# Optimization experiments

Measured on AMD Instinct MI355X. Metric: run time of the kernel, lower is better.

The kernel has to match this reference:

```python
import jax, jax.numpy as jnp
import numpy as np

GAM1 = 1.0
GAM2 = 1.0
EPS = 0.01


def setup_inputs() -> dict:
    key = jax.random.key(0)
    kx, ky = jax.random.split(key)
    m, p, k = 16384, 512, 10
    X = jax.random.normal(kx, (m, p), dtype=jnp.float32)
    Y = jax.random.randint(ky, (m,), 0, k, dtype=jnp.int64)
    return {"X": X, "Y": Y, "num_classes": k}


def reference(X, Y, num_classes):
    # W: [p, m] (features x samples), as in the torch module (W = X.T)
    W = X.reshape(X.shape[0], -1).T
    p, m = W.shape
    I = jnp.eye(p, dtype=W.dtype)

    # ---- empirical discriminative loss ----
    scalar = p / (m * EPS)
    G = W @ W.T  # [p, p]
    discrimn = jnp.linalg.slogdet(I + GAM1 * scalar * G)[1] / 2.0

    # ---- empirical compressive loss ----
    # Pi[j] is diagonal with the one-hot membership of class j, so
    # W @ Pi[j] @ W.T == (W * mask_j) @ W.T. Build all k masked Grams at once.
    M = jax.nn.one_hot(Y, num_classes, dtype=W.dtype)  # [m, k]
    trPi = M.sum(axis=0) + 1e-8                         # [k] class counts
    # Gk[j] = sum_{i in class j} w_i w_i^T  -> [k, p, p]
    Gk = jnp.einsum('pm,mk,qm->kpq', W, M, W)
    scal = (p / (trPi * EPS))[:, None, None]
    logdets = jnp.linalg.slogdet(I[None] + scal * Gk)[1]  # [k]
    compress = jnp.sum(logdets * trPi / m) / 2.0

    return (discrimn, compress)
```

## Files before the change

### kernel.cpp

```cpp
#include <hip/hip_runtime.h>
#include <math.h>

#define P 512
#define KC 10
#define NB 32
#define EPSV 0.01f
#define TR_ROWS 448
#define XT 17024
#define MSTRIDE 40

typedef __attribute__((ext_vector_type(8))) __bf16 bf16x8;
typedef __attribute__((ext_vector_type(4))) float floatx4;

__device__ __forceinline__ float rdl(float x, int l){
  return __builtin_bit_cast(float, __builtin_amdgcn_readlane(__builtin_bit_cast(int, x), l));
}

__global__ __launch_bounds__(256) void sort_k(const int* __restrict__ Y, int* __restrict__ colmap,
                                              int* __restrict__ counts, int* __restrict__ off_pad, int m){
  __shared__ int cnt[KC], offp[KC + 1], cur[KC];
  int tid = threadIdx.x;
  if (tid < KC) cnt[tid] = 0;
  __syncthreads();
  for (int i = tid; i < m; i += 256){
    int y = Y[i];
    if (y >= 0 && y < KC) atomicAdd(&cnt[y], 1);
  }
  __syncthreads();
  if (tid == 0){
    int s = 0;
    for (int j = 0; j < KC; ++j){ offp[j] = s; s += ((cnt[j] + 63) >> 6) << 6; }
    offp[KC] = s;
  }
  __syncthreads();
  if (tid < KC){ cur[tid] = offp[tid]; counts[tid] = cnt[tid]; off_pad[tid] = offp[tid]; }
  if (tid == KC) off_pad[KC] = offp[KC];
  for (int i = tid; i < XT; i += 256) colmap[i] = -1;
  __syncthreads();
  for (int i = tid; i < m; i += 256){
    int y = Y[i];
    if (y >= 0 && y < KC){
      int pos = atomicAdd(&cur[y], 1);
      colmap[pos] = i;
    }
  }
}

__global__ __launch_bounds__(256) void xt_k(const float* __restrict__ X, const int* __restrict__ colmap,
                                            __bf16* __restrict__ Xhi, __bf16* __restrict__ Xlo){
  __shared__ float T[64][65];
  int c0 = blockIdx.x * 64;
  int f0 = blockIdx.y * 64;
  int tid = threadIdx.x;

  int j = tid >> 2;
  int piece = tid & 3;
  int s = colmap[c0 + j];
  if (s >= 0){
    const float* src = X + (long)s * P + f0 + piece * 16;
    #pragma unroll
    for (int q = 0; q < 4; ++q){
      float4 v = *(const float4*)(src + q * 4);
      T[piece * 16 + q * 4 + 0][j] = v.x;
      T[piece * 16 + q * 4 + 1][j] = v.y;
      T[piece * 16 + q * 4 + 2][j] = v.z;
      T[piece * 16 + q * 4 + 3][j] = v.w;
    }
  } else {
    #pragma unroll
    for (int q = 0; q < 16; ++q) T[piece * 16 + q][j] = 0.f;
  }
  __syncthreads();

  int f = tid >> 2;
  int cp = (tid & 3) * 16;
  bf16x8 vh0, vl0, vh1, vl1;
  #pragma unroll
  for (int q = 0; q < 8; ++q){
    float x0 = T[f][cp + q];
    float x1 = T[f][cp + 8 + q];
    __bf16 h0 = (__bf16)x0, h1 = (__bf16)x1;
    vh0[q] = h0; vl0[q] = (__bf16)(x0 - (float)h0);
    vh1[q] = h1; vl1[q] = (__bf16)(x1 - (float)h1);
  }
  long base = (long)(f0 + f) * XT + c0 + cp;
  *(bf16x8*)&Xhi[base]     = vh0;
  *(bf16x8*)&Xhi[base + 8] = vh1;
  *(bf16x8*)&Xlo[base]     = vl0;
  *(bf16x8*)&Xlo[base + 8] = vl1;
}

__global__ __launch_bounds__(256) void gram_mfma(const __bf16* __restrict__ Xhi,
                                                 const __bf16* __restrict__ Xlo,
                                                 const int* __restrict__ counts,
                                                 const int* __restrict__ off_pad,
                                                 float* __restrict__ Gk){
  int cls = blockIdx.y;
  int ta = 0, rem = blockIdx.x;
  while (rem >= ta + 1){ rem -= ta + 1; ++ta; }
  int tb = rem;
  int a0 = ta * 64, b0 = tb * 64;

  int tid  = threadIdx.x;
  int lane = tid & 63;
  int wv   = tid >> 6;
  int wrow = wv >> 1, wcol = wv & 1;
  int fr   = lane & 15;
  int quad = lane >> 4;

  int cs0     = off_pad[cls];
  int nchunks = (counts[cls] + 31) >> 5;

  long arow0 = (long)(a0 + wrow * 32 + fr) * XT;
  long brow0 = (long)(b0 + wcol * 32 + fr) * XT;

  floatx4 acc[2][2];
  #pragma unroll
  for (int i = 0; i < 2; ++i)
    #pragma unroll
    for (int j = 0; j < 2; ++j) acc[i][j] = (floatx4){0.f, 0.f, 0.f, 0.f};

  for (int ch = 0; ch < nchunks; ++ch){
    long co = cs0 + ch * 32 + quad * 8;
    bf16x8 ah[2], al[2], bh[2], bl[2];
    #pragma unroll
    for (int r = 0; r < 2; ++r){
      ah[r] = *(const bf16x8*)&Xhi[arow0 + (long)r * 16 * XT + co];
      al[r] = *(const bf16x8*)&Xlo[arow0 + (long)r * 16 * XT + co];
      bh[r] = *(const bf16x8*)&Xhi[brow0 + (long)r * 16 * XT + co];
      bl[r] = *(const bf16x8*)&Xlo[brow0 + (long)r * 16 * XT + co];
    }
    #pragma unroll
    for (int ri = 0; ri < 2; ++ri)
      #pragma unroll
      for (int rj = 0; rj < 2; ++rj){
        acc[ri][rj] = __builtin_amdgcn_mfma_f32_16x16x32_bf16(al[ri], bh[rj], acc[ri][rj], 0, 0, 0);
        acc[ri][rj] = __builtin_amdgcn_mfma_f32_16x16x32_bf16(ah[ri], bl[rj], acc[ri][rj], 0, 0, 0);
        acc[ri][rj] = __builtin_amdgcn_mfma_f32_16x16x32_bf16(ah[ri], bh[rj], acc[ri][rj], 0, 0, 0);
      }
  }

  float* C = Gk + (long)cls * P * P;
  #pragma unroll
  for (int ri = 0; ri < 2; ++ri){
    int a = a0 + wrow * 32 + ri * 16 + (lane >> 4) * 4;
    #pragma unroll
    for (int rj = 0; rj < 2; ++rj){
      int b = b0 + wcol * 32 + rj * 16 + (lane & 15);
      #pragma unroll
      for (int r = 0; r < 4; ++r)
        C[(long)(a + r) * P + b] = acc[ri][rj][r];
    }
  }
}

__global__ __launch_bounds__(256) void sum10_k(float* __restrict__ Gk){
  long i = (long)blockIdx.x * 256 + threadIdx.x;
  float4 s = {0.f, 0.f, 0.f, 0.f};
  #pragma unroll
  for (int j = 0; j < KC; ++j){
    float4 v = ((const float4*)(Gk + (long)j * P * P))[i];
    s.x += v.x; s.y += v.y; s.z += v.z; s.w += v.w;
  }
  ((float4*)(Gk + (long)KC * P * P))[i] = s;
}

__global__ __launch_bounds__(512, 2) void chol_mfma(float* __restrict__ Gk,
                                                    const int* __restrict__ counts,
                                                    float* __restrict__ logdets,
                                                    float m_tot){
  __shared__ __align__(16) __bf16 Lhi[TR_ROWS * 32];
  __shared__ __align__(16) __bf16 Llo[TR_ROWS * 32];
  __shared__ __align__(16) __bf16 Mhi[NB * MSTRIDE];
  __shared__ __align__(16) __bf16 Mlo[NB * MSTRIDE];

  int mat  = blockIdx.x;
  int tid  = threadIdx.x;
  int lane = tid & 63;
  int wv   = tid >> 6;
  float* A = Gk + (long)mat * P * P;
  float sc = (mat < KC) ? ((float)P / (((float)counts[mat] + 1e-8f) * EPSV))
                        : ((float)P / (m_tot * EPSV));
  float logsum = 0.f;

  for (int s = 0; s < 16; ++s){
    int j0 = s * NB;
    int qt = P - j0 - NB;

    if (wv == 0){
      float a[NB];
      float dri[NB];
      if (lane < NB){
        const float* src = A + (long)(j0 + lane) * P + j0;
        #pragma unroll
        for (int u = 0; u < NB; u += 4){
          float4 v = *(const float4*)(src + u);
          a[u] = v.x; a[u+1] = v.y; a[u+2] = v.z; a[u+3] = v.w;
        }
        if (s == 0){
          #pragma unroll
          for (int u = 0; u < NB; ++u) a[u] *= sc;
          a[lane] += 1.0f;
        }
      } else {
        #pragma unroll
        for (int u = 0; u < NB; ++u) a[u] = 0.f;
      }
      #pragma unroll
      for (int jj = 0; jj < NB; ++jj){
        float d = rdl(a[jj], jj);
        logsum += __log2f(d);
        float inv = 1.0f / d;
        float rs  = rsqrtf(d);
        dri[jj] = rs;
        float w = a[jj] * inv;
        #pragma unroll
        for (int l = jj + 1; l < NB; ++l){
          float prl = rdl(a[l], jj);
          a[l] = fmaf(-w, prl, a[l]);
        }
        a[jj] *= rs;
      }
      float mcol[NB];
      #pragma unroll
      for (int u = 0; u < NB; ++u) mcol[u] = 0.f;
      #pragma unroll
      for (int r = 0; r < NB; ++r){
        float ssum = (lane == r) ? 1.0f : 0.0f;
        #pragma unroll
        for (int u = 0; u < r; ++u){
          float lru = rdl(a[u], r);
          ssum = fmaf(-lru, mcol[u], ssum);
        }
        mcol[r] = ssum * dri[r];
      }
      if (lane < NB){
        #pragma unroll
        for (int u = 0; u < NB; ++u){
          float f = mcol[u];
          __bf16 h = (__bf16)f;
          Mhi[u * MSTRIDE + lane] = h;
          Mlo[u * MSTRIDE + lane] = (__bf16)(f - (float)h);
        }
      }
    }
    __syncthreads();

    if (qt > 0){
      int ntiles = qt >> 4;
      int r16 = lane & 15;
      int kq  = lane >> 4;
      for (int rt = wv; rt < ntiles; rt += 8){
        int row = j0 + NB + rt * 16 + r16;
        const float* src = A + (long)row * P + j0 + kq * 8;
        float4 v0 = *(const float4*)(src);
        float4 v1 = *(const float4*)(src + 4);
        float f[8] = {v0.x, v0.y, v0.z, v0.w, v1.x, v1.y, v1.z, v1.w};
        if (s == 0){
          #pragma unroll
          for (int u = 0; u < 8; ++u) f[u] *= sc;
        }
        bf16x8 ahi, alo;
        #pragma unroll
        for (int u = 0; u < 8; ++u){
          __bf16 h = (__bf16)f[u];
          ahi[u] = h;
          alo[u] = (__bf16)(f[u] - (float)h);
        }
        #pragma unroll
        for (int ng = 0; ng < 2; ++ng){
          int mrow = ng * 16 + r16;
          bf16x8 bhi = *(const bf16x8*)&Mhi[mrow * MSTRIDE + kq * 8];
          bf16x8 blo = *(const bf16x8*)&Mlo[mrow * MSTRIDE + kq * 8];
          floatx4 acc = {0.f, 0.f, 0.f, 0.f};
          acc = __builtin_amdgcn_mfma_f32_16x16x32_bf16(alo, bhi, acc, 0, 0, 0);
          acc = __builtin_amdgcn_mfma_f32_16x16x32_bf16(ahi, blo, acc, 0, 0, 0);
          acc = __builtin_amdgcn_mfma_f32_16x16x32_bf16(ahi, bhi, acc, 0, 0, 0);
          #pragma unroll
          for (int r = 0; r < 4; ++r){
            int t  = rt * 16 + kq * 4 + r;
            int cc = ng * 16 + r16;
            int e  = (t * 4 + ((cc >> 3) ^ ((t >> 1) & 3))) * 8 + (cc & 7);
            float fv = acc[r];
            __bf16 h = (__bf16)fv;
            Lhi[e] = h;
            Llo[e] = (__bf16)(fv - (float)h);
          }
        }
      }
    }
    __syncthreads();

    if (qt > 0){
      int tt = qt >> 5;
      int T  = tt * (tt + 1) / 2;
      int trail0 = j0 + NB;
      for (int idx = wv; idx < T; idx += 8){
        int ti = 0, rem = idx;
        while (rem >= ti + 1){ rem -= ti + 1; ++ti; }
        int tj = rem;
        int I0 = ti * 32, J0 = tj * 32;
        int c  = lane >> 4;

        bf16x8 ahi2[2], alo2[2], bhi2[2], blo2[2];
        #pragma unroll
        for (int h = 0; h < 2; ++h){
          int r1 = I0 + h * 16 + (lane & 15);
          int sw1 = (r1 * 4 + (c ^ ((r1 >> 1) & 3))) * 8;
          ahi2[h] = *(const bf16x8*)&Lhi[sw1];
          alo2[h] = *(const bf16x8*)&Llo[sw1];
          int r2 = J0 + h * 16 + (lane & 15);
          int sw2 = (r2 * 4 + (c ^ ((r2 >> 1) & 3))) * 8;
          bhi2[h] = *(const bf16x8*)&Lhi[sw2];
          blo2[h] = *(const bf16x8*)&Llo[sw2];
        }

        #pragma unroll
        for (int hi_ = 0; hi_ < 2; ++hi_){
          #pragma unroll
          for (int hj = 0; hj < 2; ++hj){
            floatx4 acc = {0.f, 0.f, 0.f, 0.f};
            acc = __builtin_amdgcn_mfma_f32_16x16x32_bf16(alo2[hi_], bhi2[hj], acc, 0, 0, 0);
            acc = __builtin_amdgcn_mfma_f32_16x16x32_bf16(ahi2[hi_], blo2[hj], acc, 0, 0, 0);
            acc = __builtin_amdgcn_mfma_f32_16x16x32_bf16(ahi2[hi_], bhi2[hj], acc, 0, 0, 0);
            int grow0 = trail0 + I0 + hi_ * 16 + (lane >> 4) * 4;
            int gcol  = trail0 + J0 + hj  * 16 + (lane & 15);
            #pragma unroll
            for (int r = 0; r < 4; ++r){
              long off = (long)(grow0 + r) * P + gcol;
              float v = A[off];
              if (s == 0) v = sc * v + ((grow0 + r) == gcol ? 1.f : 0.f);
              A[off] = v - acc[r];
            }
          }
        }
      }
    }
    __syncthreads();
  }

  if (tid == 0) logdets[mat] = logsum * 0.6931471805599453f;
}

__global__ __launch_bounds__(64) void final_k(const float* __restrict__ logdets,
                                              const int* __restrict__ counts,
                                              float* __restrict__ out, float m_tot){
  if (threadIdx.x == 0 && blockIdx.x == 0){
    out[0] = 0.5f * logdets[KC];
    float comp = 0.f;
    for (int j = 0; j < KC; ++j){
      float trPi = (float)counts[j] + 1e-8f;
      comp += logdets[j] * trPi / m_tot;
    }
    out[1] = 0.5f * comp;
  }
}

extern "C" void kernel_launch(void* const* d_in, const int* in_sizes, int n_in,
                              void* d_out, int out_size, void* d_ws, size_t ws_size,
                              hipStream_t stream) {
  (void)n_in; (void)out_size; (void)ws_size;
  const float* X = (const float*)d_in[0];
  const int*   Y = (const int*)d_in[1];
  int m = in_sizes[0] / P;

  float*  Gk      = (float*)d_ws;
  __bf16* Xhi     = (__bf16*)(Gk + 11L * P * P);
  __bf16* Xlo     = Xhi + (long)P * XT;
  int*    colmap  = (int*)(Xlo + (long)P * XT);
  int*    counts  = colmap + XT;
  int*    off_pad = counts + 16;
  float*  logdets = (float*)(off_pad + 17);

  sort_k<<<1, 256, 0, stream>>>(Y, colmap, counts, off_pad, m);

  dim3 xg(XT / 64, 8);
  xt_k<<<xg, 256, 0, stream>>>(X, colmap, Xhi, Xlo);

  dim3 gg(36, KC);
  gram_mfma<<<gg, 256, 0, stream>>>(Xhi, Xlo, counts, off_pad, Gk);

  sum10_k<<<P * P / 1024, 256, 0, stream>>>(Gk);

  chol_mfma<<<KC + 1, 512, 0, stream>>>(Gk, counts, logdets, (float)m);

  final_k<<<1, 64, 0, stream>>>(logdets, counts, (float*)d_out, (float)m);
}
```

Measured before the change: 503.3 us.

## Split blocked Cholesky into per-step panel and multi-block trailing update kernels

The single-kernel blocked Cholesky, which ran one workgroup per matrix, is replaced by a host loop over 16 steps. Each step launches a panel kernel that factors the diagonal block and computes the panel L into a global bf16 hi/lo scratch, then a trailing-update kernel that spreads the symmetric rank-32 update over 8 workgroups per matrix. This lifts parallelism from 11 workgroups to 88 for the dominant trailing update. In exchange it adds about 31 kernel launches, moves the panel through global memory instead of LDS, drops the LDS swizzle, and accumulates log-determinants across launches in a global buffer.

Result: slower. 530.5 us (+5.4%).

```diff
diff --git a/kernel.cpp b/kernel.cpp
--- a/kernel.cpp
+++ b/kernel.cpp
@@ -8,6 +8,7 @@
 #define TR_ROWS 448
 #define XT 17024
 #define MSTRIDE 40
+#define NBLK 8
 
 typedef __attribute__((ext_vector_type(8))) __bf16 bf16x8;
 typedef __attribute__((ext_vector_type(4))) float floatx4;
@@ -17,10 +18,12 @@
 }
 
 __global__ __launch_bounds__(256) void sort_k(const int* __restrict__ Y, int* __restrict__ colmap,
-                                              int* __restrict__ counts, int* __restrict__ off_pad, int m){
+                                              int* __restrict__ counts, int* __restrict__ off_pad,
+                                              float* __restrict__ logacc, int m){
   __shared__ int cnt[KC], offp[KC + 1], cur[KC];
   int tid = threadIdx.x;
   if (tid < KC) cnt[tid] = 0;
+  if (tid < 16) logacc[tid] = 0.f;
   __syncthreads();
   for (int i = tid; i < m; i += 256){
     int y = Y[i];
@@ -165,12 +168,11 @@
   ((float4*)(Gk + (long)KC * P * P))[i] = s;
 }
 
-__global__ __launch_bounds__(512, 2) void chol_mfma(float* __restrict__ Gk,
-                                                    const int* __restrict__ counts,
-                                                    float* __restrict__ logdets,
-                                                    float m_tot){
-  __shared__ __align__(16) __bf16 Lhi[TR_ROWS * 32];
-  __shared__ __align__(16) __bf16 Llo[TR_ROWS * 32];
+__global__ __launch_bounds__(512, 2) void panel_k(float* __restrict__ Gk,
+                                                  const int* __restrict__ counts,
+                                                  float* __restrict__ logacc,
+                                                  __bf16* __restrict__ Lsc,
+                                                  float m_tot, int s){
   __shared__ __align__(16) __bf16 Mhi[NB * MSTRIDE];
   __shared__ __align__(16) __bf16 Mlo[NB * MSTRIDE];
 
@@ -179,48 +181,51 @@
   int lane = tid & 63;
   int wv   = tid >> 6;
   float* A = Gk + (long)mat * P * P;
+  __bf16* Lh = Lsc + (long)mat * 2 * TR_ROWS * 32;
+  __bf16* Ll = Lh + TR_ROWS * 32;
   float sc = (mat < KC) ? ((float)P / (((float)counts[mat] + 1e-8f) * EPSV))
                         : ((float)P / (m_tot * EPSV));
-  float logsum = 0.f;
-
-  for (int s = 0; s < 16; ++s){
-    int j0 = s * NB;
-    int qt = P - j0 - NB;
-
-    if (wv == 0){
-      float a[NB];
-      float dri[NB];
-      if (lane < NB){
-        const float* src = A + (long)(j0 + lane) * P + j0;
-        #pragma unroll
-        for (int u = 0; u < NB; u += 4){
-          float4 v = *(const float4*)(src + u);
-          a[u] = v.x; a[u+1] = v.y; a[u+2] = v.z; a[u+3] = v.w;
-        }
-        if (s == 0){
-          #pragma unroll
-          for (int u = 0; u < NB; ++u) a[u] *= sc;
-          a[lane] += 1.0f;
-        }
-      } else {
-        #pragma unroll
-        for (int u = 0; u < NB; ++u) a[u] = 0.f;
-      }
-      #pragma unroll
-      for (int jj = 0; jj < NB; ++jj){
-        float d = rdl(a[jj], jj);
-        logsum += __log2f(d);
-        float inv = 1.0f / d;
-        float rs  = rsqrtf(d);
-        dri[jj] = rs;
-        float w = a[jj] * inv;
-        #pragma unroll
-        for (int l = jj + 1; l < NB; ++l){
-          float prl = rdl(a[l], jj);
-          a[l] = fmaf(-w, prl, a[l]);
-        }
-        a[jj] *= rs;
-      }
+
+  int j0 = s * NB;
+  int qt = P - j0 - NB;
+
+  if (wv == 0){
+    float a[NB];
+    float dri[NB];
+    float logsum = 0.f;
+    if (lane < NB){
+      const float* src = A + (long)(j0 + lane) * P + j0;
+      #pragma unroll
+      for (int u = 0; u < NB; u += 4){
+        float4 v = *(const float4*)(src + u);
+        a[u] = v.x; a[u+1] = v.y; a[u+2] = v.z; a[u+3] = v.w;
+      }
+      if (s == 0){
+        #pragma unroll
+        for (int u = 0; u < NB; ++u) a[u] *= sc;
+        a[lane] += 1.0f;
+      }
+    } else {
+      #pragma unroll
+      for (int u = 0; u < NB; ++u) a[u] = 0.f;
+    }
+    #pragma unroll
+    for (int jj = 0; jj < NB; ++jj){
+      float d = rdl(a[jj], jj);
+      logsum += __log2f(d);
+      float inv = 1.0f / d;
+      float rs  = rsqrtf(d);
+      dri[jj] = rs;
+      float w = a[jj] * inv;
+      #pragma unroll
+      for (int l = jj + 1; l < NB; ++l){
+        float prl = rdl(a[l], jj);
+        a[l] = fmaf(-w, prl, a[l]);
+      }
+      a[jj] *= rs;
+    }
+    if (lane == 0) logacc[mat] += logsum;
+    if (qt > 0){
       float mcol[NB];
       #pragma unroll
       for (int u = 0; u < NB; ++u) mcol[u] = 0.f;
@@ -244,113 +249,126 @@
         }
       }
     }
-    __syncthreads();
-
-    if (qt > 0){
-      int ntiles = qt >> 4;
-      int r16 = lane & 15;
-      int kq  = lane >> 4;
-      for (int rt = wv; rt < ntiles; rt += 8){
-        int row = j0 + NB + rt * 16 + r16;
-        const float* src = A + (long)row * P + j0 + kq * 8;
-        float4 v0 = *(const float4*)(src);
-        float4 v1 = *(const float4*)(src + 4);
-        float f[8] = {v0.x, v0.y, v0.z, v0.w, v1.x, v1.y, v1.z, v1.w};
-        if (s == 0){
-          #pragma unroll
-          for (int u = 0; u < 8; ++u) f[u] *= sc;
+  }
+  __syncthreads();
+
+  if (qt > 0){
+    int ntiles = qt >> 4;
+    int r16 = lane & 15;
+    int kq  = lane >> 4;
+    for (int rt = wv; rt < ntiles; rt += 8){
+      int row = j0 + NB + rt * 16 + r16;
+      const float* src = A + (long)row * P + j0 + kq * 8;
+      float4 v0 = *(const float4*)(src);
+      float4 v1 = *(const float4*)(src + 4);
+      float f[8] = {v0.x, v0.y, v0.z, v0.w, v1.x, v1.y, v1.z, v1.w};
+      if (s == 0){
+        #pragma unroll
+        for (int u = 0; u < 8; ++u) f[u] *= sc;
+      }
+      bf16x8 ahi, alo;
+      #pragma unroll
+      for (int u = 0; u < 8; ++u){
+        __bf16 h = (__bf16)f[u];
+        ahi[u] = h;
+        alo[u] = (__bf16)(f[u] - (float)h);
+      }
+      #pragma unroll
+      for (int ng = 0; ng < 2; ++ng){
+        int mrow = ng * 16 + r16;
+        bf16x8 bhi = *(const bf16x8*)&Mhi[mrow * MSTRIDE + kq * 8];
+        bf16x8 blo = *(const bf16x8*)&Mlo[mrow * MSTRIDE + kq * 8];
+        floatx4 acc = {0.f, 0.f, 0.f, 0.f};
+        acc = __builtin_amdgcn_mfma_f32_16x16x32_bf16(alo, bhi, acc, 0, 0, 0);
+        acc = __builtin_amdgcn_mfma_f32_16x16x32_bf16(ahi, blo, acc, 0, 0, 0);
+        acc = __builtin_amdgcn_mfma_f32_16x16x32_bf16(ahi, bhi, acc, 0, 0, 0);
+        #pragma unroll
+        for (int r = 0; r < 4; ++r){
+          int t  = rt * 16 + kq * 4 + r;
+          int cc = ng * 16 + r16;
+          float fv = acc[r];
+          __bf16 h = (__bf16)fv;
+          Lh[t * 32 + cc] = h;
+          Ll[t * 32 + cc] = (__bf16)(fv - (float)h);
         }
-        bf16x8 ahi, alo;
-        #pragma unroll
-        for (int u = 0; u < 8; ++u){
-          __bf16 h = (__bf16)f[u];
-          ahi[u] = h;
-          alo[u] = (__bf16)(f[u] - (float)h);
+      }
+    }
+  }
+}
+
+__global__ __launch_bounds__(512, 2) void trail_k(float* __restrict__ Gk,
+                                                  const __bf16* __restrict__ Lsc,
+                                                  const int* __restrict__ counts,
+                                                  float m_tot, int s){
+  int mat = blockIdx.x / NBLK;
+  int blk = blockIdx.x % NBLK;
+  int tid  = threadIdx.x;
+  int lane = tid & 63;
+  int wv   = tid >> 6;
+  int gw   = blk * 8 + wv;
+  float* A = Gk + (long)mat * P * P;
+  const __bf16* Lh = Lsc + (long)mat * 2 * TR_ROWS * 32;
+  const __bf16* Ll = Lh + TR_ROWS * 32;
+  float sc = (mat < KC) ? ((float)P / (((float)counts[mat] + 1e-8f) * EPSV))
+                        : ((float)P / (m_tot * EPSV));
+
+  int j0 = s * NB;
+  int qt = P - j0 - NB;
+  if (qt <= 0) return;
+  int tt = qt >> 5;
+  int T  = tt * (tt + 1) / 2;
+  int trail0 = j0 + NB;
+  int c = lane >> 4;
+
+  for (int idx = gw; idx < T; idx += NBLK * 8){
+    int ti = 0, rem = idx;
+    while (rem >= ti + 1){ rem -= ti + 1; ++ti; }
+    int tj = rem;
+    int I0 = ti * 32, J0 = tj * 32;
+
+    bf16x8 ahi2[2], alo2[2], bhi2[2], blo2[2];
+    #pragma unroll
+    for (int h = 0; h < 2; ++h){
+      int r1 = I0 + h * 16 + (lane & 15);
+      ahi2[h] = *(const bf16x8*)&Lh[r1 * 32 + c * 8];
+      alo2[h] = *(const bf16x8*)&Ll[r1 * 32 + c * 8];
+      int r2 = J0 + h * 16 + (lane & 15);
+      bhi2[h] = *(const bf16x8*)&Lh[r2 * 32 + c * 8];
+      blo2[h] = *(const bf16x8*)&Ll[r2 * 32 + c * 8];
+    }
+
+    #pragma unroll
+    for (int hi_ = 0; hi_ < 2; ++hi_){
+      #pragma unroll
+      for (int hj = 0; hj < 2; ++hj){
+        floatx4 acc = {0.f, 0.f, 0.f, 0.f};
+        acc = __builtin_amdgcn_mfma_f32_16x16x32_bf16(alo2[hi_], bhi2[hj], acc, 0, 0, 0);
+        acc = __builtin_amdgcn_mfma_f32_16x16x32_bf16(ahi2[hi_], blo2[hj], acc, 0, 0, 0);
+        acc = __builtin_amdgcn_mfma_f32_16x16x32_bf16(ahi2[hi_], bhi2[hj], acc, 0, 0, 0);
+        int grow0 = trail0 + I0 + hi_ * 16 + (lane >> 4) * 4;
+        int gcol  = trail0 + J0 + hj  * 16 + (lane & 15);
+        #pragma unroll
+        for (int r = 0; r < 4; ++r){
+          long off = (long)(grow0 + r) * P + gcol;
+          float v = A[off];
+          if (s == 0) v = sc * v + ((grow0 + r) == gcol ? 1.f : 0.f);
+          A[off] = v - acc[r];
         }
-        #pragma unroll
-        for (int ng = 0; ng < 2; ++ng){
-          int mrow = ng * 16 + r16;
-          bf16x8 bhi = *(const bf16x8*)&Mhi[mrow * MSTRIDE + kq * 8];
-          bf16x8 blo = *(const bf16x8*)&Mlo[mrow * MSTRIDE + kq * 8];
-          floatx4 acc = {0.f, 0.f, 0.f, 0.f};
-          acc = __builtin_amdgcn_mfma_f32_16x16x32_bf16(alo, bhi, acc, 0, 0, 0);
-          acc = __builtin_amdgcn_mfma_f32_16x16x32_bf16(ahi, blo, acc, 0, 0, 0);
-          acc = __builtin_amdgcn_mfma_f32_16x16x32_bf16(ahi, bhi, acc, 0, 0, 0);
-          #pragma unroll
-          for (int r = 0; r < 4; ++r){
-            int t  = rt * 16 + kq * 4 + r;
-            int cc = ng * 16 + r16;
-            int e  = (t * 4 + ((cc >> 3) ^ ((t >> 1) & 3))) * 8 + (cc & 7);
-            float fv = acc[r];
-            __bf16 h = (__bf16)fv;
-            Lhi[e] = h;
-            Llo[e] = (__bf16)(fv - (float)h);
-          }
-        }
-      }
-    }
-    __syncthreads();
-
-    if (qt > 0){
-      int tt = qt >> 5;
-      int T  = tt * (tt + 1) / 2;
-      int trail0 = j0 + NB;
-      for (int idx = wv; idx < T; idx += 8){
-        int ti = 0, rem = idx;
-        while (rem >= ti + 1){ rem -= ti + 1; ++ti; }
-        int tj = rem;
-        int I0 = ti * 32, J0 = tj * 32;
-        int c  = lane >> 4;
-
-        bf16x8 ahi2[2], alo2[2], bhi2[2], blo2[2];
-        #pragma unroll
-        for (int h = 0; h < 2; ++h){
-          int r1 = I0 + h * 16 + (lane & 15);
-          int sw1 = (r1 * 4 + (c ^ ((r1 >> 1) & 3))) * 8;
-          ahi2[h] = *(const bf16x8*)&Lhi[sw1];
-          alo2[h] = *(const bf16x8*)&Llo[sw1];
-          int r2 = J0 + h * 16 + (lane & 15);
-          int sw2 = (r2 * 4 + (c ^ ((r2 >> 1) & 3))) * 8;
-          bhi2[h] = *(const bf16x8*)&Lhi[sw2];
-          blo2[h] = *(const bf16x8*)&Llo[sw2];
-        }
-
-        #pragma unroll
-        for (int hi_ = 0; hi_ < 2; ++hi_){
-          #pragma unroll
-          for (int hj = 0; hj < 2; ++hj){
-            floatx4 acc = {0.f, 0.f, 0.f, 0.f};
-            acc = __builtin_amdgcn_mfma_f32_16x16x32_bf16(alo2[hi_], bhi2[hj], acc, 0, 0, 0);
-            acc = __builtin_amdgcn_mfma_f32_16x16x32_bf16(ahi2[hi_], blo2[hj], acc, 0, 0, 0);
-            acc = __builtin_amdgcn_mfma_f32_16x16x32_bf16(ahi2[hi_], bhi2[hj], acc, 0, 0, 0);
-            int grow0 = trail0 + I0 + hi_ * 16 + (lane >> 4) * 4;
-            int gcol  = trail0 + J0 + hj  * 16 + (lane & 15);
-            #pragma unroll
-            for (int r = 0; r < 4; ++r){
-              long off = (long)(grow0 + r) * P + gcol;
-              float v = A[off];
-              if (s == 0) v = sc * v + ((grow0 + r) == gcol ? 1.f : 0.f);
-              A[off] = v - acc[r];
-            }
-          }
-        }
-      }
-    }
-    __syncthreads();
-  }
-
-  if (tid == 0) logdets[mat] = logsum * 0.6931471805599453f;
-}
-
-__global__ __launch_bounds__(64) void final_k(const float* __restrict__ logdets,
+      }
+    }
+  }
+}
+
+__global__ __launch_bounds__(64) void final_k(const float* __restrict__ logacc,
                                               const int* __restrict__ counts,
                                               float* __restrict__ out, float m_tot){
   if (threadIdx.x == 0 && blockIdx.x == 0){
-    out[0] = 0.5f * logdets[KC];
+    const float LN2 = 0.6931471805599453f;
+    out[0] = 0.5f * logacc[KC] * LN2;
     float comp = 0.f;
     for (int j = 0; j < KC; ++j){
       float trPi = (float)counts[j] + 1e-8f;
-      comp += logdets[j] * trPi / m_tot;
+      comp += logacc[j] * LN2 * trPi / m_tot;
     }
     out[1] = 0.5f * comp;
   }
@@ -370,9 +388,10 @@
   int*    colmap  = (int*)(Xlo + (long)P * XT);
   int*    counts  = colmap + XT;
   int*    off_pad = counts + 16;
-  float*  logdets = (float*)(off_pad + 17);
-
-  sort_k<<<1, 256, 0, stream>>>(Y, colmap, counts, off_pad, m);
+  float*  logacc  = (float*)(off_pad + 20);
+  __bf16* Lsc     = (__bf16*)(logacc + 16);
+
+  sort_k<<<1, 256, 0, stream>>>(Y, colmap, counts, off_pad, logacc, m);
 
   dim3 xg(XT / 64, 8);
   xt_k<<<xg, 256, 0, stream>>>(X, colmap, Xhi, Xlo);
@@ -382,7 +401,11 @@
 
   sum10_k<<<P * P / 1024, 256, 0, stream>>>(Gk);
 
-  chol_mfma<<<KC + 1, 512, 0, stream>>>(Gk, counts, logdets, (float)m);
-
-  final_k<<<1, 64, 0, stream>>>(logdets, counts, (float*)d_out, (float)m);
-}
+  for (int s = 0; s < 16; ++s){
+    panel_k<<<KC + 1, 512, 0, stream>>>(Gk, counts, logacc, Lsc, (float)m, s);
+    if (s < 15)
+      trail_k<<<(KC + 1) * NBLK, 512, 0, stream>>>(Gk, Lsc, counts, (float)m, s);
+  }
+
+  final_k<<<1, 64, 0, stream>>>(logacc, counts, (float*)d_out, (float)m);
+}
```
